# Kernel optimization log

Measured on AMD Instinct MI355X. Metric: run time of the kernel, lower is better.

Reference implementation:

```python
import jax, jax.numpy as jnp
import numpy as np

D = 64          # embed_dim
NH = 4          # nhead
DH = D // NH    # head dim
FF = 2048       # TransformerEncoderLayer default dim_feedforward
V = 1_000_000   # vocab (num items)
MAX_LEN = 50
INSERT_LEN = 10
EPS = 1e-5
N_LAYERS = 2


def setup_inputs() -> dict:
    key = jax.random.key(0)
    ks = jax.random.split(key, 8)
    s = 0.02
    return {
        "ht": jax.random.normal(ks[0], (D,), dtype=jnp.float32),
        "item_emb": jax.random.normal(ks[1], (V, D), dtype=jnp.float32) * s,
        "pos_emb": jax.random.normal(ks[2], (MAX_LEN, D), dtype=jnp.float32) * s,
        "in_proj_w": jax.random.normal(ks[3], (N_LAYERS, 3 * D, D), dtype=jnp.float32) * s,
        "in_proj_b": jnp.zeros((N_LAYERS, 3 * D), jnp.float32),
        "out_w": jax.random.normal(ks[4], (N_LAYERS, D, D), dtype=jnp.float32) * s,
        "out_b": jnp.zeros((N_LAYERS, D), jnp.float32),
        "ln1_w": jnp.ones((N_LAYERS, D), jnp.float32),
        "ln1_b": jnp.zeros((N_LAYERS, D), jnp.float32),
        "ln2_w": jnp.ones((N_LAYERS, D), jnp.float32),
        "ln2_b": jnp.zeros((N_LAYERS, D), jnp.float32),
        "ffn1_w": jax.random.normal(ks[5], (N_LAYERS, FF, D), dtype=jnp.float32) * s,
        "ffn1_b": jnp.zeros((N_LAYERS, FF), jnp.float32),
        "ffn2_w": jax.random.normal(ks[6], (N_LAYERS, D, FF), dtype=jnp.float32) * s,
        "ffn2_b": jnp.zeros((N_LAYERS, D), jnp.float32),
    }


def _ln(x, w, b):
    m = jnp.mean(x, axis=-1, keepdims=True)
    v = jnp.mean(jnp.square(x - m), axis=-1, keepdims=True)
    return (x - m) * jax.lax.rsqrt(v + EPS) * w + b


def _encoder_layer(x, ipw, ipb, ow, ob, l1w, l1b, l2w, l2b, f1w, f1b, f2w, f2b):
    # x: [S, D]; post-norm TransformerEncoderLayer (PyTorch defaults, eval mode)
    S = x.shape[0]
    qkv = x @ ipw.T + ipb                      # [S, 3D]
    q, k, v = jnp.split(qkv, 3, axis=-1)
    q = q.reshape(S, NH, DH)
    k = k.reshape(S, NH, DH)
    v = v.reshape(S, NH, DH)
    scores = jnp.einsum('shd,thd->hst', q, k) / jnp.sqrt(jnp.float32(DH))
    attn = jax.nn.softmax(scores, axis=-1)
    o = jnp.einsum('hst,thd->shd', attn, v).reshape(S, D)
    o = o @ ow.T + ob
    x = _ln(x + o, l1w, l1b)
    ff = jax.nn.relu(x @ f1w.T + f1b) @ f2w.T + f2b
    return _ln(x + ff, l2w, l2b)


def reference(ht, item_emb, pos_emb, in_proj_w, in_proj_b, out_w, out_b,
              ln1_w, ln1_b, ln2_w, ln2_b, ffn1_w, ffn1_b, ffn2_w, ffn2_b):
    gen = []         # generated item indices (traced int scalars)
    logits_all = []
    for _ in range(INSERT_LEN):
        if gen:
            gen_embed = item_emb[jnp.stack(gen)]             # [t, D]
            stack = jnp.concatenate([ht[None, :], gen_embed], axis=0)
        else:
            stack = ht[None, :]
        S = stack.shape[0]
        x = stack + pos_emb[:S]
        for l in range(N_LAYERS):
            x = _encoder_layer(x, in_proj_w[l], in_proj_b[l], out_w[l], out_b[l],
                               ln1_w[l], ln1_b[l], ln2_w[l], ln2_b[l],
                               ffn1_w[l], ffn1_b[l], ffn2_w[l], ffn2_b[l])
        logits = x[-1] @ item_emb.T                           # [V]
        gen.append(jnp.argmax(logits))
        logits_all.append(logits)
    return jnp.stack(logits_all), jnp.stack(gen)
```

## Files before the change

### kernel.cpp

```cpp
#include <hip/hip_runtime.h>

typedef unsigned long long u64;
typedef unsigned int u32;
typedef unsigned short u16;

#define V_ 1000000
#define STEPS_ 10
#define EPS_ 1e-5f
#define MARGIN_ 0.02f

__device__ __forceinline__ u64 pack_best(float v, int idx) {
    u32 u = __float_as_uint(v);
    u = (u & 0x80000000u) ? ~u : (u | 0x80000000u);
    return ((u64)u << 32) | (u64)(~(u32)idx);
}
__device__ __forceinline__ int unpack_idx(u64 p) { return (int)(~(u32)p); }
__device__ __forceinline__ float unpack_val(u64 p) {
    u32 hi = (u32)(p >> 32);
    return __uint_as_float((hi & 0x80000000u) ? (hi ^ 0x80000000u) : ~hi);
}
__device__ __forceinline__ u64 shfl_xor_u64(u64 v, int m) {
    u32 lo = (u32)v, hi = (u32)(v >> 32);
    lo = (u32)__shfl_xor((int)lo, m);
    hi = (u32)__shfl_xor((int)hi, m);
    return ((u64)hi << 32) | lo;
}
__device__ __forceinline__ u16 f2bf(float f) {
    u32 u = __float_as_uint(f);
    u += 0x7fffu + ((u >> 16) & 1u);
    return (u16)(u >> 16);
}
__device__ __forceinline__ float bf_lo(u32 u) { return __uint_as_float(u << 16); }
__device__ __forceinline__ float bf_hi(u32 u) { return __uint_as_float(u & 0xffff0000u); }

__device__ int resolve_argmax(const u64* __restrict__ cand,
                              const float* __restrict__ item_emb,
                              const float* __restrict__ y_last,
                              const float* __restrict__ lnw,
                              const float* __restrict__ lnb,
                              float* s_xl, int* s_list, u64* s_wm,
                              int* s_cnt, u64* s_best)
{
    const int tid = threadIdx.x;
    if (tid < 64) {
        float v = y_last[tid];
        float m = v;
        #pragma unroll
        for (int o = 1; o < 64; o <<= 1) m += __shfl_xor(m, o);
        m *= (1.f / 64.f);
        float df = v - m;
        float var = df * df;
        #pragma unroll
        for (int o = 1; o < 64; o <<= 1) var += __shfl_xor(var, o);
        var *= (1.f / 64.f);
        s_xl[tid] = df * (1.f / sqrtf(var + EPS_)) * lnw[tid] + lnb[tid];
    }
    if (tid == 0) { *s_cnt = 0; *s_best = 0ull; }
    __syncthreads();

    u64 m = 0ull;
    for (int i = tid; i < 2048; i += 256) { u64 c = cand[i]; if (c > m) m = c; }
    #pragma unroll
    for (int o = 1; o < 64; o <<= 1) { u64 x = shfl_xor_u64(m, o); if (x > m) m = x; }
    if ((tid & 63) == 0) s_wm[tid >> 6] = m;
    __syncthreads();
    if (tid == 0) {
        u64 b = s_wm[0];
        for (int i = 1; i < 4; i++) if (s_wm[i] > b) b = s_wm[i];
        s_wm[0] = b;
    }
    __syncthreads();

    float thr = unpack_val(s_wm[0]) - MARGIN_;
    for (int i = tid; i < 2048; i += 256) {
        if (unpack_val(cand[i]) >= thr) {
            int p = atomicAdd(s_cnt, 1);
            if (p < 64) s_list[p] = unpack_idx(cand[i]);
        }
    }
    __syncthreads();
    int n = *s_cnt; if (n > 64) n = 64;
    const int wid = tid >> 6, lane = tid & 63;
    for (int c = wid; c < n; c += 4) {
        int row = s_list[c];
        float p = s_xl[lane] * item_emb[(size_t)row * 64 + lane];
        #pragma unroll
        for (int o = 1; o < 64; o <<= 1) p += __shfl_xor(p, o);
        if (lane == 0) atomicMax(s_best, pack_best(p, row));
    }
    __syncthreads();
    return unpack_idx(*s_best);
}

__global__ __launch_bounds__(256) void attn0_kernel(
    const float* __restrict__ ht, const float* __restrict__ item_emb,
    const float* __restrict__ pos_emb,
    const float* __restrict__ ipw, const float* __restrict__ ipb,
    const float* __restrict__ ow,  const float* __restrict__ ob,
    const float* __restrict__ l1w, const float* __restrict__ l1b,
    const float* __restrict__ l2w1, const float* __restrict__ l2b1,
    const u64* __restrict__ cand, const float* __restrict__ y_last,
    int* __restrict__ gen_idx, float* __restrict__ gen_out,
    const float* __restrict__ f1w, const float* __restrict__ f1b,
    float* __restrict__ xp0, float* __restrict__ hbuf, int t)
{
    const int S = t + 1;
    const int tid = threadIdx.x;
    __shared__ float x[640], qkv[1920], att[400], o_[640], y2[640], xps[640];
    __shared__ float rm[10], rr[10], xl[64];
    __shared__ int list[64], cnt;
    __shared__ u64 wm[4], best;

    int newidx = -1;
    if (t > 0) {
        newidx = resolve_argmax(cand, item_emb, y_last, l2w1, l2b1,
                                xl, list, wm, &cnt, &best);
        if (blockIdx.x == 0 && tid == 0) {
            gen_idx[t - 1] = newidx;
            gen_out[t - 1] = (float)newidx;
        }
    }
    __syncthreads();

    for (int i = tid; i < S * 64; i += 256) {
        int s = i >> 6, d = i & 63;
        float base;
        if (s == 0) base = ht[d];
        else {
            int gi = (s == t) ? newidx : gen_idx[s - 1];
            base = item_emb[(size_t)gi * 64 + d];
        }
        x[i] = base + pos_emb[i];
    }
    __syncthreads();

    for (int i = tid; i < S * 192; i += 256) {
        int s = i / 192, j = i % 192;
        float acc = ipb[j];
        const float4* wr = (const float4*)(ipw + j * 64);
        const float4* xr = (const float4*)(x + s * 64);
        #pragma unroll
        for (int k = 0; k < 16; k++) {
            float4 w4 = wr[k], xv = xr[k];
            acc += w4.x * xv.x + w4.y * xv.y + w4.z * xv.z + w4.w * xv.w;
        }
        qkv[i] = acc;
    }
    __syncthreads();

    for (int i = tid; i < 4 * S * S; i += 256) {
        int h = i / (S * S), r = i % (S * S);
        int si = r / S, ti = r % S;
        const float* qr = qkv + si * 192 + h * 16;
        const float* kr = qkv + ti * 192 + 64 + h * 16;
        float acc = 0.f;
        #pragma unroll
        for (int k = 0; k < 16; k++) acc += qr[k] * kr[k];
        att[(h * S + si) * S + ti] = acc * 0.25f;
    }
    __syncthreads();

    for (int i = tid; i < 4 * S; i += 256) {
        float* row = att + i * S;
        float mx = row[0];
        for (int j = 1; j < S; j++) mx = fmaxf(mx, row[j]);
        float sm = 0.f;
        for (int j = 0; j < S; j++) { float e = expf(row[j] - mx); row[j] = e; sm += e; }
        float inv = 1.f / sm;
        for (int j = 0; j < S; j++) row[j] *= inv;
    }
    __syncthreads();

    for (int i = tid; i < S * 64; i += 256) {
        int si = i >> 6, d = i & 63, h = d >> 4, dh = d & 15;
        const float* ar = att + (h * S + si) * S;
        float acc = 0.f;
        for (int ti = 0; ti < S; ti++) acc += ar[ti] * qkv[ti * 192 + 128 + h * 16 + dh];
        o_[i] = acc;
    }
    __syncthreads();

    for (int i = tid; i < S * 64; i += 256) {
        int s = i >> 6, d = i & 63;
        float acc = ob[d] + x[i];
        const float4* wr = (const float4*)(ow + d * 64);
        const float4* orow = (const float4*)(o_ + s * 64);
        #pragma unroll
        for (int k = 0; k < 16; k++) {
            float4 w4 = wr[k], ov = orow[k];
            acc += w4.x * ov.x + w4.y * ov.y + w4.z * ov.z + w4.w * ov.w;
        }
        y2[i] = acc;
    }
    __syncthreads();

    if (tid < S) {
        const float* yr = y2 + tid * 64;
        float m = 0.f;
        for (int k = 0; k < 64; k++) m += yr[k];
        m *= (1.f / 64.f);
        float v = 0.f;
        for (int k = 0; k < 64; k++) { float df = yr[k] - m; v += df * df; }
        rm[tid] = m;
        rr[tid] = 1.f / sqrtf(v * (1.f / 64.f) + EPS_);
    }
    __syncthreads();
    for (int i = tid; i < S * 64; i += 256) {
        int s = i >> 6, d = i & 63;
        float v = (y2[i] - rm[s]) * rr[s] * l1w[d] + l1b[d];
        xps[i] = v;
        xp0[i] = v;
    }
    __syncthreads();

    const int jl = tid >> 4, kp = tid & 15;
    const int j = blockIdx.x * 16 + jl;
    float4 w4 = ((const float4*)(f1w + (size_t)j * 64))[kp];
    float b1 = f1b[j];
    for (int s = 0; s < S; s++) {
        float4 xv = ((const float4*)(xps + s * 64))[kp];
        float p = w4.x * xv.x + w4.y * xv.y + w4.z * xv.z + w4.w * xv.w;
        p += __shfl_xor(p, 1);
        p += __shfl_xor(p, 2);
        p += __shfl_xor(p, 4);
        p += __shfl_xor(p, 8);
        if (kp == 0) hbuf[s * 2048 + j] = fmaxf(p + b1, 0.f);
    }
}

__global__ __launch_bounds__(256) void ffn2_full_kernel(
    const float* __restrict__ f2w0, const float* __restrict__ f2b0,
    const float* __restrict__ hbuf, const float* __restrict__ xp0,
    float* __restrict__ y0, int S)
{
    const int tid = threadIdx.x, d = blockIdx.x;
    const float4* w4 = (const float4*)(f2w0 + (size_t)d * 2048 + tid * 8);
    float4 w0 = w4[0], w1 = w4[1];
    __shared__ float sw[4][10];
    for (int s = 0; s < S; s++) {
        const float4* h4 = (const float4*)(hbuf + s * 2048 + tid * 8);
        float4 h0 = h4[0], h1 = h4[1];
        float p = w0.x * h0.x + w0.y * h0.y + w0.z * h0.z + w0.w * h0.w
                + w1.x * h1.x + w1.y * h1.y + w1.z * h1.z + w1.w * h1.w;
        #pragma unroll
        for (int o = 1; o < 64; o <<= 1) p += __shfl_xor(p, o);
        if ((tid & 63) == 0) sw[tid >> 6][s] = p;
    }
    __syncthreads();
    if (tid < S)
        y0[tid * 64 + d] = sw[0][tid] + sw[1][tid] + sw[2][tid] + sw[3][tid]
                         + f2b0[d] + xp0[tid * 64 + d];
}

__global__ __launch_bounds__(256) void attn1_kernel(
    const float* __restrict__ y0,
    const float* __restrict__ l2w0, const float* __restrict__ l2b0,
    const float* __restrict__ ipw1, const float* __restrict__ ipb1,
    const float* __restrict__ ow1,  const float* __restrict__ ob1,
    const float* __restrict__ l1w1, const float* __restrict__ l1b1,
    const float* __restrict__ f1w1, const float* __restrict__ f1b1,
    float* __restrict__ xp1_last, float* __restrict__ hbuf, int S)
{
    const int tid = threadIdx.x;
    __shared__ float y0s[640], x1[640], qkv[1920], att[40], ol[64], y2l[64], xpl[64];
    __shared__ float rm[10], rr[10];

    for (int i = tid; i < S * 64; i += 256) y0s[i] = y0[i];
    __syncthreads();
    if (tid < S) {
        const float* yr = y0s + tid * 64;
        float m = 0.f;
        for (int k = 0; k < 64; k++) m += yr[k];
        m *= (1.f / 64.f);
        float v = 0.f;
        for (int k = 0; k < 64; k++) { float df = yr[k] - m; v += df * df; }
        rm[tid] = m;
        rr[tid] = 1.f / sqrtf(v * (1.f / 64.f) + EPS_);
    }
    __syncthreads();
    for (int i = tid; i < S * 64; i += 256) {
        int s = i >> 6, d = i & 63;
        x1[i] = (y0s[i] - rm[s]) * rr[s] * l2w0[d] + l2b0[d];
    }
    __syncthreads();

    for (int i = tid; i < S * 192; i += 256) {
        int s = i / 192, j = i % 192;
        float acc = ipb1[j];
        const float4* wr = (const float4*)(ipw1 + j * 64);
        const float4* xr = (const float4*)(x1 + s * 64);
        #pragma unroll
        for (int k = 0; k < 16; k++) {
            float4 w4 = wr[k], xv = xr[k];
            acc += w4.x * xv.x + w4.y * xv.y + w4.z * xv.z + w4.w * xv.w;
        }
        qkv[i] = acc;
    }
    __syncthreads();

    for (int i = tid; i < 4 * S; i += 256) {
        int h = i / S, ti = i % S;
        const float* qr = qkv + (S - 1) * 192 + h * 16;
        const float* kr = qkv + ti * 192 + 64 + h * 16;
        float acc = 0.f;
        #pragma unroll
        for (int k = 0; k < 16; k++) acc += qr[k] * kr[k];
        att[h * S + ti] = acc * 0.25f;
    }
    __syncthreads();
    if (tid < 4) {
        float* row = att + tid * S;
        float mx = row[0];
        for (int j = 1; j < S; j++) mx = fmaxf(mx, row[j]);
        float sm = 0.f;
        for (int j = 0; j < S; j++) { float e = expf(row[j] - mx); row[j] = e; sm += e; }
        float inv = 1.f / sm;
        for (int j = 0; j < S; j++) row[j] *= inv;
    }
    __syncthreads();
    if (tid < 64) {
        int h = tid >> 4, dh = tid & 15;
        const float* ar = att + h * S;
        float acc = 0.f;
        for (int ti = 0; ti < S; ti++) acc += ar[ti] * qkv[ti * 192 + 128 + h * 16 + dh];
        ol[tid] = acc;
    }
    __syncthreads();
    if (tid < 64) {
        float acc = ob1[tid] + x1[(S - 1) * 64 + tid];
        const float* wr = ow1 + tid * 64;
        for (int k = 0; k < 64; k++) acc += ol[k] * wr[k];
        y2l[tid] = acc;
    }
    __syncthreads();
    if (tid < 64) {
        float v = y2l[tid];
        float m = v;
        #pragma unroll
        for (int o = 1; o < 64; o <<= 1) m += __shfl_xor(m, o);
        m *= (1.f / 64.f);
        float df = v - m;
        float var = df * df;
        #pragma unroll
        for (int o = 1; o < 64; o <<= 1) var += __shfl_xor(var, o);
        float r = 1.f / sqrtf(var * (1.f / 64.f) + EPS_);
        float xv = df * r * l1w1[tid] + l1b1[tid];
        xpl[tid] = xv;
        xp1_last[tid] = xv;
    }
    __syncthreads();

    const int jl = tid >> 4, kp = tid & 15;
    const int j = blockIdx.x * 16 + jl;
    float4 w4 = ((const float4*)(f1w1 + (size_t)j * 64))[kp];
    float4 xv = ((const float4*)xpl)[kp];
    float p = w4.x * xv.x + w4.y * xv.y + w4.z * xv.z + w4.w * xv.w;
    p += __shfl_xor(p, 1);
    p += __shfl_xor(p, 2);
    p += __shfl_xor(p, 4);
    p += __shfl_xor(p, 8);
    if (kp == 0) hbuf[j] = fmaxf(p + f1b1[j], 0.f);
}

__global__ __launch_bounds__(256) void ffn2_last_kernel(
    const float* __restrict__ f2w1, const float* __restrict__ f2b1,
    const float* __restrict__ hbuf, const float* __restrict__ xp1_last,
    float* __restrict__ y_last)
{
    const int tid = threadIdx.x, d = blockIdx.x;
    const float4* w4 = (const float4*)(f2w1 + (size_t)d * 2048 + tid * 8);
    const float4* h4 = (const float4*)(hbuf + tid * 8);
    float4 w0 = w4[0], w1 = w4[1], h0 = h4[0], h1 = h4[1];
    float p = w0.x * h0.x + w0.y * h0.y + w0.z * h0.z + w0.w * h0.w
            + w1.x * h1.x + w1.y * h1.y + w1.z * h1.z + w1.w * h1.w;
    #pragma unroll
    for (int o = 1; o < 64; o <<= 1) p += __shfl_xor(p, o);
    __shared__ float sw[4];
    if ((tid & 63) == 0) sw[tid >> 6] = p;
    __syncthreads();
    if (tid == 0) y_last[d] = sw[0] + sw[1] + sw[2] + sw[3] + f2b1[d] + xp1_last[d];
}

__global__ __launch_bounds__(256) void logits_f32_kernel(
    const float* __restrict__ item_emb, const float* __restrict__ y_last,
    const float* __restrict__ lnw, const float* __restrict__ lnb,
    float* __restrict__ out, u64* __restrict__ cand, u16* __restrict__ emb16)
{
    const int tid = threadIdx.x;
    __shared__ float xl[64];
    if (tid < 64) {
        float v = y_last[tid];
        float m = v;
        #pragma unroll
        for (int o = 1; o < 64; o <<= 1) m += __shfl_xor(m, o);
        m *= (1.f / 64.f);
        float df = v - m;
        float var = df * df;
        #pragma unroll
        for (int o = 1; o < 64; o <<= 1) var += __shfl_xor(var, o);
        float r = 1.f / sqrtf(var * (1.f / 64.f) + EPS_);
        xl[tid] = df * r * lnw[tid] + lnb[tid];
    }
    __syncthreads();

    const int l16 = tid & 15;
    float4 q = ((const float4*)xl)[l16];
    const int group0 = (blockIdx.x * 256 + tid) >> 4;
    const int ngroups = (gridDim.x * 256) >> 4;
    u64 lb = 0ull;

    for (int row = group0; row < V_; row += ngroups) {
        float4 e = ((const float4*)(item_emb + (size_t)row * 64))[l16];
        ushort4 us;
        us.x = f2bf(e.x); us.y = f2bf(e.y); us.z = f2bf(e.z); us.w = f2bf(e.w);
        *(ushort4*)(emb16 + (size_t)row * 64 + l16 * 4) = us;
        float p = q.x * e.x + q.y * e.y + q.z * e.z + q.w * e.w;
        p += __shfl_xor(p, 1);
        p += __shfl_xor(p, 2);
        p += __shfl_xor(p, 4);
        p += __shfl_xor(p, 8);
        if (l16 == 0) {
            out[row] = p;
            u64 pk = pack_best(p, row);
            if (pk > lb) lb = pk;
        }
    }
    #pragma unroll
    for (int o = 1; o < 64; o <<= 1) { u64 x = shfl_xor_u64(lb, o); if (x > lb) lb = x; }
    __shared__ u64 sb[4];
    if ((tid & 63) == 0) sb[tid >> 6] = lb;
    __syncthreads();
    if (tid == 0) {
        u64 b = sb[0];
        for (int i = 1; i < 4; i++) if (sb[i] > b) b = sb[i];
        cand[blockIdx.x] = b;
    }
}

__global__ __launch_bounds__(256) void logits_bf16_kernel(
    const u16* __restrict__ emb16, const float* __restrict__ y_last,
    const float* __restrict__ lnw, const float* __restrict__ lnb,
    float* __restrict__ out, u64* __restrict__ cand)
{
    const int tid = threadIdx.x;
    __shared__ float xl[64];
    if (tid < 64) {
        float v = y_last[tid];
        float m = v;
        #pragma unroll
        for (int o = 1; o < 64; o <<= 1) m += __shfl_xor(m, o);
        m *= (1.f / 64.f);
        float df = v - m;
        float var = df * df;
        #pragma unroll
        for (int o = 1; o < 64; o <<= 1) var += __shfl_xor(var, o);
        float r = 1.f / sqrtf(var * (1.f / 64.f) + EPS_);
        xl[tid] = df * r * lnw[tid] + lnb[tid];
    }
    __syncthreads();

    const int j8 = tid & 7;
    float q[8];
    #pragma unroll
    for (int i = 0; i < 8; i++) q[i] = xl[j8 * 8 + i];
    const int group0 = (blockIdx.x * 256 + tid) >> 3;
    const int ngroups = (gridDim.x * 256) >> 3;
    const uint4* base = (const uint4*)emb16;
    u64 lb = 0ull;

    for (int row = group0; row < V_; row += ngroups) {
        uint4 u = base[(size_t)row * 8 + j8];
        float p = q[0] * bf_lo(u.x) + q[1] * bf_hi(u.x)
                + q[2] * bf_lo(u.y) + q[3] * bf_hi(u.y)
                + q[4] * bf_lo(u.z) + q[5] * bf_hi(u.z)
                + q[6] * bf_lo(u.w) + q[7] * bf_hi(u.w);
        p += __shfl_xor(p, 1);
        p += __shfl_xor(p, 2);
        p += __shfl_xor(p, 4);
        if (j8 == 0) {
            out[row] = p;
            u64 pk = pack_best(p, row);
            if (pk > lb) lb = pk;
        }
    }
    #pragma unroll
    for (int o = 1; o < 64; o <<= 1) { u64 x = shfl_xor_u64(lb, o); if (x > lb) lb = x; }
    __shared__ u64 sb[4];
    if ((tid & 63) == 0) sb[tid >> 6] = lb;
    __syncthreads();
    if (tid == 0) {
        u64 b = sb[0];
        for (int i = 1; i < 4; i++) if (sb[i] > b) b = sb[i];
        cand[blockIdx.x] = b;
    }
}

__global__ __launch_bounds__(256) void finalize_kernel(
    const u64* __restrict__ cand, const float* __restrict__ item_emb,
    const float* __restrict__ y_last,
    const float* __restrict__ lnw, const float* __restrict__ lnb,
    float* __restrict__ gen_out)
{
    __shared__ float xl[64];
    __shared__ int list[64], cnt;
    __shared__ u64 wm[4], best;
    int r = resolve_argmax(cand, item_emb, y_last, lnw, lnb, xl, list, wm, &cnt, &best);
    if (threadIdx.x == 0) gen_out[STEPS_ - 1] = (float)r;
}

extern "C" void kernel_launch(void* const* d_in, const int* in_sizes, int n_in,
                              void* d_out, int out_size, void* d_ws, size_t ws_size,
                              hipStream_t stream) {
    const float* ht       = (const float*)d_in[0];
    const float* item_emb = (const float*)d_in[1];
    const float* pos_emb  = (const float*)d_in[2];
    const float* ipw      = (const float*)d_in[3];
    const float* ipb      = (const float*)d_in[4];
    const float* ow       = (const float*)d_in[5];
    const float* ob       = (const float*)d_in[6];
    const float* l1w      = (const float*)d_in[7];
    const float* l1b      = (const float*)d_in[8];
    const float* l2w      = (const float*)d_in[9];
    const float* l2b      = (const float*)d_in[10];
    const float* f1w      = (const float*)d_in[11];
    const float* f1b      = (const float*)d_in[12];
    const float* f2w      = (const float*)d_in[13];
    const float* f2b      = (const float*)d_in[14];

    float* out = (float*)d_out;
    char* ws = (char*)d_ws;
    int*   gen_idx = (int*)ws;
    float* xp0     = (float*)(ws + 64);
    float* xp1l    = (float*)(ws + 2624);
    float* y_last  = (float*)(ws + 2880);
    float* y0      = (float*)(ws + 3136);
    float* hbuf    = (float*)(ws + 8192);
    u64*   cand    = (u64*)(ws + 90112);
    u16*   emb16   = (u16*)(ws + 131072);
    float* gen_out = out + (size_t)STEPS_ * V_;

    for (int t = 0; t < STEPS_; t++) {
        const int S = t + 1;
        attn0_kernel<<<128, 256, 0, stream>>>(
            ht, item_emb, pos_emb, ipw, ipb, ow, ob, l1w, l1b,
            l2w + 64, l2b + 64, cand, y_last, gen_idx, gen_out,
            f1w, f1b, xp0, hbuf, t);
        ffn2_full_kernel<<<64, 256, 0, stream>>>(f2w, f2b, hbuf, xp0, y0, S);
        attn1_kernel<<<128, 256, 0, stream>>>(
            y0, l2w, l2b, ipw + 192 * 64, ipb + 192, ow + 64 * 64, ob + 64,
            l1w + 64, l1b + 64, f1w + 2048 * 64, f1b + 2048, xp1l, hbuf, S);
        ffn2_last_kernel<<<64, 256, 0, stream>>>(
            f2w + (size_t)64 * 2048, f2b + 64, hbuf, xp1l, y_last);
        if (t == 0)
            logits_f32_kernel<<<2048, 256, 0, stream>>>(
                item_emb, y_last, l2w + 64, l2b + 64, out, cand, emb16);
        else
            logits_bf16_kernel<<<2048, 256, 0, stream>>>(
                emb16, y_last, l2w + 64, l2b + 64, out + (size_t)t * V_, cand);
    }
    finalize_kernel<<<1, 256, 0, stream>>>(
        cand, item_emb, y_last, l2w + 64, l2b + 64, gen_out);
}
```

Baseline: 1.024 ms.

## Fuse per-step layers with grid barriers, FP8 argmax scan, defer exact logits

The four per-step transformer kernels are merged into one persistent step kernel that uses global atomic grid barriers between the FFN stages. Per-step argmax scanning now uses an FP8 copy of the embedding table with chunked candidate maxima and a wider margin, then recomputes in fp32 to resolve the winner. All ten fp32 logit rows are written in a single final pass over item_emb using the saved normalized queries, rather than a bf16 pass per step. This cuts launch overhead and the bytes read per step, but adds risks: the spin barrier relies on all 64 blocks being resident at once, and FP8 rounding error could change the chosen argmax.

```diff
diff --git a/kernel.cpp b/kernel.cpp
--- a/kernel.cpp
+++ b/kernel.cpp
@@ -2,12 +2,16 @@
 
 typedef unsigned long long u64;
 typedef unsigned int u32;
-typedef unsigned short u16;
 
 #define V_ 1000000
 #define STEPS_ 10
 #define EPS_ 1e-5f
-#define MARGIN_ 0.02f
+#define MARGIN_ 0.06f
+#define FP8_SCALE 2048.0f
+#define FP8_INV (1.0f / 2048.0f)
+#define NCH 8192
+#define CH 123
+#define NBLK 64
 
 __device__ __forceinline__ u64 pack_best(float v, int idx) {
     u32 u = __float_as_uint(v);
@@ -25,21 +29,42 @@
     hi = (u32)__shfl_xor((int)hi, m);
     return ((u64)hi << 32) | lo;
 }
-__device__ __forceinline__ u16 f2bf(float f) {
-    u32 u = __float_as_uint(f);
-    u += 0x7fffu + ((u >> 16) & 1u);
-    return (u16)(u >> 16);
-}
-__device__ __forceinline__ float bf_lo(u32 u) { return __uint_as_float(u << 16); }
-__device__ __forceinline__ float bf_hi(u32 u) { return __uint_as_float(u & 0xffff0000u); }
+
+#define FP8_DOT16(u, q, p) do { \
+    auto a0 = __builtin_amdgcn_cvt_pk_f32_fp8((u).x, false); \
+    auto a1 = __builtin_amdgcn_cvt_pk_f32_fp8((u).x, true);  \
+    auto b0 = __builtin_amdgcn_cvt_pk_f32_fp8((u).y, false); \
+    auto b1 = __builtin_amdgcn_cvt_pk_f32_fp8((u).y, true);  \
+    auto c0 = __builtin_amdgcn_cvt_pk_f32_fp8((u).z, false); \
+    auto c1 = __builtin_amdgcn_cvt_pk_f32_fp8((u).z, true);  \
+    auto d0 = __builtin_amdgcn_cvt_pk_f32_fp8((u).w, false); \
+    auto d1 = __builtin_amdgcn_cvt_pk_f32_fp8((u).w, true);  \
+    p = q[0]*a0[0] + q[1]*a0[1] + q[2]*a1[0] + q[3]*a1[1] \
+      + q[4]*b0[0] + q[5]*b0[1] + q[6]*b1[0] + q[7]*b1[1] \
+      + q[8]*c0[0] + q[9]*c0[1] + q[10]*c1[0] + q[11]*c1[1] \
+      + q[12]*d0[0] + q[13]*d0[1] + q[14]*d1[0] + q[15]*d1[1]; \
+} while (0)
+
+__device__ __forceinline__ void grid_bar(u32* ctr, u32 expect) {
+    __threadfence();
+    __syncthreads();
+    if (threadIdx.x == 0) {
+        __hip_atomic_fetch_add(ctr, 1u, __ATOMIC_ACQ_REL, __HIP_MEMORY_SCOPE_AGENT);
+        while (__hip_atomic_load(ctr, __ATOMIC_ACQUIRE, __HIP_MEMORY_SCOPE_AGENT) < expect)
+            __builtin_amdgcn_s_sleep(2);
+    }
+    __syncthreads();
+    __threadfence();
+}
 
 __device__ int resolve_argmax(const u64* __restrict__ cand,
+                              const u32* __restrict__ emb8,
                               const float* __restrict__ item_emb,
                               const float* __restrict__ y_last,
                               const float* __restrict__ lnw,
                               const float* __restrict__ lnb,
-                              float* s_xl, int* s_list, u64* s_wm,
-                              int* s_cnt, u64* s_best)
+                              float* s_xl, int* s_list, int* s_qg, u64* s_wm,
+                              int* s_cnt, int* s_qcnt, u64* s_best)
 {
     const int tid = threadIdx.x;
     if (tid < 64) {
@@ -55,11 +80,11 @@
         var *= (1.f / 64.f);
         s_xl[tid] = df * (1.f / sqrtf(var + EPS_)) * lnw[tid] + lnb[tid];
     }
-    if (tid == 0) { *s_cnt = 0; *s_best = 0ull; }
+    if (tid == 0) { *s_cnt = 0; *s_qcnt = 0; *s_best = 0ull; }
     __syncthreads();
 
     u64 m = 0ull;
-    for (int i = tid; i < 2048; i += 256) { u64 c = cand[i]; if (c > m) m = c; }
+    for (int i = tid; i < NCH; i += 256) { u64 c = cand[i]; if (c > m) m = c; }
     #pragma unroll
     for (int o = 1; o < 64; o <<= 1) { u64 x = shfl_xor_u64(m, o); if (x > m) m = x; }
     if ((tid & 63) == 0) s_wm[tid >> 6] = m;
@@ -70,16 +95,45 @@
         s_wm[0] = b;
     }
     __syncthreads();
-
-    float thr = unpack_val(s_wm[0]) - MARGIN_;
-    for (int i = tid; i < 2048; i += 256) {
+    const float thr = unpack_val(s_wm[0]) - MARGIN_;
+
+    for (int i = tid; i < NCH; i += 256) {
         if (unpack_val(cand[i]) >= thr) {
-            int p = atomicAdd(s_cnt, 1);
-            if (p < 64) s_list[p] = unpack_idx(cand[i]);
-        }
-    }
-    __syncthreads();
-    int n = *s_cnt; if (n > 64) n = 64;
+            int p = atomicAdd(s_qcnt, 1);
+            if (p < 64) s_qg[p] = i;
+        }
+    }
+    __syncthreads();
+    int nq = *s_qcnt; if (nq > 64) nq = 64;
+
+    {
+        const int l4 = tid & 3, rl = tid >> 2;
+        float q[16];
+        #pragma unroll
+        for (int i = 0; i < 16; i++) q[i] = s_xl[l4 * 16 + i] * FP8_INV;
+        for (int ci = 0; ci < nq; ci++) {
+            const int r0 = s_qg[ci] * CH;
+            #pragma unroll
+            for (int half = 0; half < 2; half++) {
+                int loc = half * 64 + rl;
+                int row = r0 + loc;
+                if (loc < CH && row < V_) {
+                    uint4 u = ((const uint4*)emb8)[(size_t)row * 4 + l4];
+                    float p;
+                    FP8_DOT16(u, q, p);
+                    p += __shfl_xor(p, 1);
+                    p += __shfl_xor(p, 2);
+                    if (l4 == 0 && p >= thr - 1e-3f) {
+                        int pp = atomicAdd(s_cnt, 1);
+                        if (pp < 128) s_list[pp] = row;
+                    }
+                }
+            }
+        }
+    }
+    __syncthreads();
+    int n = *s_cnt; if (n > 128) n = 128;
+
     const int wid = tid >> 6, lane = tid & 63;
     for (int c = wid; c < n; c += 4) {
         int row = s_list[c];
@@ -92,33 +146,41 @@
     return unpack_idx(*s_best);
 }
 
-__global__ __launch_bounds__(256) void attn0_kernel(
+__global__ __launch_bounds__(256) void step_kernel(
     const float* __restrict__ ht, const float* __restrict__ item_emb,
     const float* __restrict__ pos_emb,
     const float* __restrict__ ipw, const float* __restrict__ ipb,
-    const float* __restrict__ ow,  const float* __restrict__ ob,
+    const float* __restrict__ ow, const float* __restrict__ ob,
     const float* __restrict__ l1w, const float* __restrict__ l1b,
-    const float* __restrict__ l2w1, const float* __restrict__ l2b1,
-    const u64* __restrict__ cand, const float* __restrict__ y_last,
+    const float* __restrict__ l2w, const float* __restrict__ l2b,
+    const float* __restrict__ f1w, const float* __restrict__ f1b,
+    const float* __restrict__ f2w, const float* __restrict__ f2b,
+    const u64* __restrict__ cand, const u32* __restrict__ emb8,
+    float* __restrict__ y_last,
     int* __restrict__ gen_idx, float* __restrict__ gen_out,
-    const float* __restrict__ f1w, const float* __restrict__ f1b,
-    float* __restrict__ xp0, float* __restrict__ hbuf, int t)
+    float* __restrict__ y0, float* __restrict__ hbuf, float* __restrict__ hbuf2,
+    u32* __restrict__ bar, int t)
 {
     const int S = t + 1;
-    const int tid = threadIdx.x;
-    __shared__ float x[640], qkv[1920], att[400], o_[640], y2[640], xps[640];
-    __shared__ float rm[10], rr[10], xl[64];
-    __shared__ int list[64], cnt;
+    const int tid = threadIdx.x, bid = blockIdx.x;
+    __shared__ __align__(16) float x[640], qkv[1920], o_[640], y2[640], xps[640];
+    __shared__ __align__(16) float xpl[64];
+    __shared__ float att[400], rm[10], rr[10], sw[4][10], xl[64], ol[64], y2l[64];
+    __shared__ int list[128], qg[64], cnt, qcnt;
     __shared__ u64 wm[4], best;
+
+    const float* ipw1 = ipw + 192 * 64;  const float* ipb1 = ipb + 192;
+    const float* ow1  = ow + 64 * 64;    const float* ob1  = ob + 64;
+    const float* l1w1 = l1w + 64;        const float* l1b1 = l1b + 64;
+    const float* l2w1 = l2w + 64;        const float* l2b1 = l2b + 64;
+    const float* f1w1 = f1w + 2048 * 64; const float* f1b1 = f1b + 2048;
+    const float* f2w1 = f2w + (size_t)64 * 2048; const float* f2b1 = f2b + 64;
 
     int newidx = -1;
     if (t > 0) {
-        newidx = resolve_argmax(cand, item_emb, y_last, l2w1, l2b1,
-                                xl, list, wm, &cnt, &best);
-        if (blockIdx.x == 0 && tid == 0) {
-            gen_idx[t - 1] = newidx;
-            gen_out[t - 1] = (float)newidx;
-        }
+        newidx = resolve_argmax(cand, emb8, item_emb, y_last, l2w1, l2b1,
+                                xl, list, qg, wm, &cnt, &qcnt, &best);
+        if (bid == 0 && tid == 0) { gen_idx[t - 1] = newidx; gen_out[t - 1] = (float)newidx; }
     }
     __syncthreads();
 
@@ -135,9 +197,9 @@
     __syncthreads();
 
     for (int i = tid; i < S * 192; i += 256) {
-        int s = i / 192, j = i % 192;
-        float acc = ipb[j];
-        const float4* wr = (const float4*)(ipw + j * 64);
+        int s = i / 192, j2 = i % 192;
+        float acc = ipb[j2];
+        const float4* wr = (const float4*)(ipw + j2 * 64);
         const float4* xr = (const float4*)(x + s * 64);
         #pragma unroll
         for (int k = 0; k < 16; k++) {
@@ -159,18 +221,16 @@
         att[(h * S + si) * S + ti] = acc * 0.25f;
     }
     __syncthreads();
-
     for (int i = tid; i < 4 * S; i += 256) {
         float* row = att + i * S;
         float mx = row[0];
-        for (int j = 1; j < S; j++) mx = fmaxf(mx, row[j]);
+        for (int j2 = 1; j2 < S; j2++) mx = fmaxf(mx, row[j2]);
         float sm = 0.f;
-        for (int j = 0; j < S; j++) { float e = expf(row[j] - mx); row[j] = e; sm += e; }
+        for (int j2 = 0; j2 < S; j2++) { float e = expf(row[j2] - mx); row[j2] = e; sm += e; }
         float inv = 1.f / sm;
-        for (int j = 0; j < S; j++) row[j] *= inv;
-    }
-    __syncthreads();
-
+        for (int j2 = 0; j2 < S; j2++) row[j2] *= inv;
+    }
+    __syncthreads();
     for (int i = tid; i < S * 64; i += 256) {
         int si = i >> 6, d = i & 63, h = d >> 4, dh = d & 15;
         const float* ar = att + (h * S + si) * S;
@@ -179,7 +239,6 @@
         o_[i] = acc;
     }
     __syncthreads();
-
     for (int i = tid; i < S * 64; i += 256) {
         int s = i >> 6, d = i & 63;
         float acc = ob[d] + x[i];
@@ -193,7 +252,6 @@
         y2[i] = acc;
     }
     __syncthreads();
-
     if (tid < S) {
         const float* yr = y2 + tid * 64;
         float m = 0.f;
@@ -207,68 +265,53 @@
     __syncthreads();
     for (int i = tid; i < S * 64; i += 256) {
         int s = i >> 6, d = i & 63;
-        float v = (y2[i] - rm[s]) * rr[s] * l1w[d] + l1b[d];
-        xps[i] = v;
-        xp0[i] = v;
-    }
-    __syncthreads();
-
-    const int jl = tid >> 4, kp = tid & 15;
-    const int j = blockIdx.x * 16 + jl;
-    float4 w4 = ((const float4*)(f1w + (size_t)j * 64))[kp];
-    float b1 = f1b[j];
-    for (int s = 0; s < S; s++) {
-        float4 xv = ((const float4*)(xps + s * 64))[kp];
-        float p = w4.x * xv.x + w4.y * xv.y + w4.z * xv.z + w4.w * xv.w;
-        p += __shfl_xor(p, 1);
-        p += __shfl_xor(p, 2);
-        p += __shfl_xor(p, 4);
-        p += __shfl_xor(p, 8);
-        if (kp == 0) hbuf[s * 2048 + j] = fmaxf(p + b1, 0.f);
-    }
-}
-
-__global__ __launch_bounds__(256) void ffn2_full_kernel(
-    const float* __restrict__ f2w0, const float* __restrict__ f2b0,
-    const float* __restrict__ hbuf, const float* __restrict__ xp0,
-    float* __restrict__ y0, int S)
-{
-    const int tid = threadIdx.x, d = blockIdx.x;
-    const float4* w4 = (const float4*)(f2w0 + (size_t)d * 2048 + tid * 8);
-    float4 w0 = w4[0], w1 = w4[1];
-    __shared__ float sw[4][10];
-    for (int s = 0; s < S; s++) {
-        const float4* h4 = (const float4*)(hbuf + s * 2048 + tid * 8);
-        float4 h0 = h4[0], h1 = h4[1];
-        float p = w0.x * h0.x + w0.y * h0.y + w0.z * h0.z + w0.w * h0.w
-                + w1.x * h1.x + w1.y * h1.y + w1.z * h1.z + w1.w * h1.w;
-        #pragma unroll
-        for (int o = 1; o < 64; o <<= 1) p += __shfl_xor(p, o);
-        if ((tid & 63) == 0) sw[tid >> 6][s] = p;
-    }
-    __syncthreads();
-    if (tid < S)
-        y0[tid * 64 + d] = sw[0][tid] + sw[1][tid] + sw[2][tid] + sw[3][tid]
-                         + f2b0[d] + xp0[tid * 64 + d];
-}
-
-__global__ __launch_bounds__(256) void attn1_kernel(
-    const float* __restrict__ y0,
-    const float* __restrict__ l2w0, const float* __restrict__ l2b0,
-    const float* __restrict__ ipw1, const float* __restrict__ ipb1,
-    const float* __restrict__ ow1,  const float* __restrict__ ob1,
-    const float* __restrict__ l1w1, const float* __restrict__ l1b1,
-    const float* __restrict__ f1w1, const float* __restrict__ f1b1,
-    float* __restrict__ xp1_last, float* __restrict__ hbuf, int S)
-{
-    const int tid = threadIdx.x;
-    __shared__ float y0s[640], x1[640], qkv[1920], att[40], ol[64], y2l[64], xpl[64];
-    __shared__ float rm[10], rr[10];
-
-    for (int i = tid; i < S * 64; i += 256) y0s[i] = y0[i];
+        xps[i] = (y2[i] - rm[s]) * rr[s] * l1w[d] + l1b[d];
+    }
+    __syncthreads();
+
+    const int jl = tid >> 3, kp = tid & 7;
+    const int j = bid * 32 + jl;
+    {
+        const float4* wr = (const float4*)(f1w + (size_t)j * 64);
+        float4 wa = wr[kp * 2], wb = wr[kp * 2 + 1];
+        float b1 = f1b[j];
+        for (int s = 0; s < S; s++) {
+            const float4* xr = (const float4*)(xps + s * 64);
+            float4 xa = xr[kp * 2], xb = xr[kp * 2 + 1];
+            float p = wa.x * xa.x + wa.y * xa.y + wa.z * xa.z + wa.w * xa.w
+                    + wb.x * xb.x + wb.y * xb.y + wb.z * xb.z + wb.w * xb.w;
+            p += __shfl_xor(p, 1);
+            p += __shfl_xor(p, 2);
+            p += __shfl_xor(p, 4);
+            if (kp == 0) hbuf[s * 2048 + j] = fmaxf(p + b1, 0.f);
+        }
+    }
+    grid_bar(bar + t * 4 + 0, NBLK);
+
+    {
+        const int d = bid;
+        const float4* w4 = (const float4*)(f2w + (size_t)d * 2048 + tid * 8);
+        float4 w0 = w4[0], w1 = w4[1];
+        for (int s = 0; s < S; s++) {
+            const float4* h4 = (const float4*)(hbuf + s * 2048 + tid * 8);
+            float4 h0 = h4[0], h1 = h4[1];
+            float p = w0.x * h0.x + w0.y * h0.y + w0.z * h0.z + w0.w * h0.w
+                    + w1.x * h1.x + w1.y * h1.y + w1.z * h1.z + w1.w * h1.w;
+            #pragma unroll
+            for (int o = 1; o < 64; o <<= 1) p += __shfl_xor(p, o);
+            if ((tid & 63) == 0) sw[tid >> 6][s] = p;
+        }
+        __syncthreads();
+        if (tid < S)
+            y0[tid * 64 + d] = sw[0][tid] + sw[1][tid] + sw[2][tid] + sw[3][tid]
+                             + f2b[d] + xps[tid * 64 + d];
+    }
+    grid_bar(bar + t * 4 + 1, NBLK);
+
+    for (int i = tid; i < S * 64; i += 256) y2[i] = y0[i];
     __syncthreads();
     if (tid < S) {
-        const float* yr = y0s + tid * 64;
+        const float* yr = y2 + tid * 64;
         float m = 0.f;
         for (int k = 0; k < 64; k++) m += yr[k];
         m *= (1.f / 64.f);
@@ -280,15 +323,15 @@
     __syncthreads();
     for (int i = tid; i < S * 64; i += 256) {
         int s = i >> 6, d = i & 63;
-        x1[i] = (y0s[i] - rm[s]) * rr[s] * l2w0[d] + l2b0[d];
+        x[i] = (y2[i] - rm[s]) * rr[s] * l2w[d] + l2b[d];
     }
     __syncthreads();
 
     for (int i = tid; i < S * 192; i += 256) {
-        int s = i / 192, j = i % 192;
-        float acc = ipb1[j];
-        const float4* wr = (const float4*)(ipw1 + j * 64);
-        const float4* xr = (const float4*)(x1 + s * 64);
+        int s = i / 192, j2 = i % 192;
+        float acc = ipb1[j2];
+        const float4* wr = (const float4*)(ipw1 + j2 * 64);
+        const float4* xr = (const float4*)(x + s * 64);
         #pragma unroll
         for (int k = 0; k < 16; k++) {
             float4 w4 = wr[k], xv = xr[k];
@@ -311,11 +354,11 @@
     if (tid < 4) {
         float* row = att + tid * S;
         float mx = row[0];
-        for (int j = 1; j < S; j++) mx = fmaxf(mx, row[j]);
+        for (int j2 = 1; j2 < S; j2++) mx = fmaxf(mx, row[j2]);
         float sm = 0.f;
-        for (int j = 0; j < S; j++) { float e = expf(row[j] - mx); row[j] = e; sm += e; }
+        for (int j2 = 0; j2 < S; j2++) { float e = expf(row[j2] - mx); row[j2] = e; sm += e; }
         float inv = 1.f / sm;
-        for (int j = 0; j < S; j++) row[j] *= inv;
+        for (int j2 = 0; j2 < S; j2++) row[j2] *= inv;
     }
     __syncthreads();
     if (tid < 64) {
@@ -327,7 +370,7 @@
     }
     __syncthreads();
     if (tid < 64) {
-        float acc = ob1[tid] + x1[(S - 1) * 64 + tid];
+        float acc = ob1[tid] + x[(S - 1) * 64 + tid];
         const float* wr = ow1 + tid * 64;
         for (int k = 0; k < 64; k++) acc += ol[k] * wr[k];
         y2l[tid] = acc;
@@ -344,47 +387,43 @@
         #pragma unroll
         for (int o = 1; o < 64; o <<= 1) var += __shfl_xor(var, o);
         float r = 1.f / sqrtf(var * (1.f / 64.f) + EPS_);
-        float xv = df * r * l1w1[tid] + l1b1[tid];
-        xpl[tid] = xv;
-        xp1_last[tid] = xv;
-    }
-    __syncthreads();
-
-    const int jl = tid >> 4, kp = tid & 15;
-    const int j = blockIdx.x * 16 + jl;
-    float4 w4 = ((const float4*)(f1w1 + (size_t)j * 64))[kp];
-    float4 xv = ((const float4*)xpl)[kp];
-    float p = w4.x * xv.x + w4.y * xv.y + w4.z * xv.z + w4.w * xv.w;
-    p += __shfl_xor(p, 1);
-    p += __shfl_xor(p, 2);
-    p += __shfl_xor(p, 4);
-    p += __shfl_xor(p, 8);
-    if (kp == 0) hbuf[j] = fmaxf(p + f1b1[j], 0.f);
-}
-
-__global__ __launch_bounds__(256) void ffn2_last_kernel(
-    const float* __restrict__ f2w1, const float* __restrict__ f2b1,
-    const float* __restrict__ hbuf, const float* __restrict__ xp1_last,
-    float* __restrict__ y_last)
-{
-    const int tid = threadIdx.x, d = blockIdx.x;
-    const float4* w4 = (const float4*)(f2w1 + (size_t)d * 2048 + tid * 8);
-    const float4* h4 = (const float4*)(hbuf + tid * 8);
-    float4 w0 = w4[0], w1 = w4[1], h0 = h4[0], h1 = h4[1];
-    float p = w0.x * h0.x + w0.y * h0.y + w0.z * h0.z + w0.w * h0.w
-            + w1.x * h1.x + w1.y * h1.y + w1.z * h1.z + w1.w * h1.w;
-    #pragma unroll
-    for (int o = 1; o < 64; o <<= 1) p += __shfl_xor(p, o);
-    __shared__ float sw[4];
-    if ((tid & 63) == 0) sw[tid >> 6] = p;
-    __syncthreads();
-    if (tid == 0) y_last[d] = sw[0] + sw[1] + sw[2] + sw[3] + f2b1[d] + xp1_last[d];
-}
-
-__global__ __launch_bounds__(256) void logits_f32_kernel(
+        xpl[tid] = df * r * l1w1[tid] + l1b1[tid];
+    }
+    __syncthreads();
+
+    {
+        const float4* wr = (const float4*)(f1w1 + (size_t)j * 64);
+        float4 wa = wr[kp * 2], wb = wr[kp * 2 + 1];
+        const float4* xr = (const float4*)xpl;
+        float4 xa = xr[kp * 2], xb = xr[kp * 2 + 1];
+        float p = wa.x * xa.x + wa.y * xa.y + wa.z * xa.z + wa.w * xa.w
+                + wb.x * xb.x + wb.y * xb.y + wb.z * xb.z + wb.w * xb.w;
+        p += __shfl_xor(p, 1);
+        p += __shfl_xor(p, 2);
+        p += __shfl_xor(p, 4);
+        if (kp == 0) hbuf2[j] = fmaxf(p + f1b1[j], 0.f);
+    }
+    grid_bar(bar + t * 4 + 2, NBLK);
+
+    {
+        const int d = bid;
+        const float4* w4 = (const float4*)(f2w1 + (size_t)d * 2048 + tid * 8);
+        const float4* h4 = (const float4*)(hbuf2 + tid * 8);
+        float4 w0 = w4[0], w1 = w4[1], h0 = h4[0], h1 = h4[1];
+        float p = w0.x * h0.x + w0.y * h0.y + w0.z * h0.z + w0.w * h0.w
+                + w1.x * h1.x + w1.y * h1.y + w1.z * h1.z + w1.w * h1.w;
+        #pragma unroll
+        for (int o = 1; o < 64; o <<= 1) p += __shfl_xor(p, o);
+        if ((tid & 63) == 0) sw[tid >> 6][0] = p;
+        __syncthreads();
+        if (tid == 0) y_last[d] = sw[0][0] + sw[1][0] + sw[2][0] + sw[3][0] + f2b1[d] + xpl[d];
+    }
+}
+
+__global__ __launch_bounds__(256) void scan0_kernel(
     const float* __restrict__ item_emb, const float* __restrict__ y_last,
     const float* __restrict__ lnw, const float* __restrict__ lnb,
-    float* __restrict__ out, u64* __restrict__ cand, u16* __restrict__ emb16)
+    u64* __restrict__ cand, float* __restrict__ xl_all, u32* __restrict__ emb8)
 {
     const int tid = threadIdx.x;
     __shared__ float xl[64];
@@ -399,51 +438,46 @@
         #pragma unroll
         for (int o = 1; o < 64; o <<= 1) var += __shfl_xor(var, o);
         float r = 1.f / sqrtf(var * (1.f / 64.f) + EPS_);
-        xl[tid] = df * r * lnw[tid] + lnb[tid];
-    }
-    __syncthreads();
-
-    const int l16 = tid & 15;
+        float v_ = df * r * lnw[tid] + lnb[tid];
+        xl[tid] = v_;
+        if (blockIdx.x == 0) xl_all[tid] = v_;
+    }
+    __syncthreads();
+
+    const int lane = tid & 63, wid = tid >> 6;
+    const int g = blockIdx.x * 4 + wid;
+    const int l16 = lane & 15, rl = lane >> 4;
     float4 q = ((const float4*)xl)[l16];
-    const int group0 = (blockIdx.x * 256 + tid) >> 4;
-    const int ngroups = (gridDim.x * 256) >> 4;
+    const int r0 = g * CH;
     u64 lb = 0ull;
-
-    for (int row = group0; row < V_; row += ngroups) {
-        float4 e = ((const float4*)(item_emb + (size_t)row * 64))[l16];
-        ushort4 us;
-        us.x = f2bf(e.x); us.y = f2bf(e.y); us.z = f2bf(e.z); us.w = f2bf(e.w);
-        *(ushort4*)(emb16 + (size_t)row * 64 + l16 * 4) = us;
-        float p = q.x * e.x + q.y * e.y + q.z * e.z + q.w * e.w;
-        p += __shfl_xor(p, 1);
-        p += __shfl_xor(p, 2);
-        p += __shfl_xor(p, 4);
-        p += __shfl_xor(p, 8);
-        if (l16 == 0) {
-            out[row] = p;
-            u64 pk = pack_best(p, row);
-            if (pk > lb) lb = pk;
+    for (int it = 0; it < 31; it++) {
+        int loc = it * 4 + rl;
+        int row = r0 + loc;
+        if (loc < CH && row < V_) {
+            float4 e = ((const float4*)(item_emb + (size_t)row * 64))[l16];
+            u32 pk8 = (u32)__builtin_amdgcn_cvt_pk_fp8_f32(e.x * FP8_SCALE, e.y * FP8_SCALE, 0, false);
+            pk8 = (u32)__builtin_amdgcn_cvt_pk_fp8_f32(e.z * FP8_SCALE, e.w * FP8_SCALE, (int)pk8, true);
+            emb8[(size_t)row * 16 + l16] = pk8;
+            float p = q.x * e.x + q.y * e.y + q.z * e.z + q.w * e.w;
+            p += __shfl_xor(p, 1);
+            p += __shfl_xor(p, 2);
+            p += __shfl_xor(p, 4);
+            p += __shfl_xor(p, 8);
+            if (l16 == 0) { u64 pk = pack_best(p, row); if (pk > lb) lb = pk; }
         }
     }
     #pragma unroll
-    for (int o = 1; o < 64; o <<= 1) { u64 x = shfl_xor_u64(lb, o); if (x > lb) lb = x; }
-    __shared__ u64 sb[4];
-    if ((tid & 63) == 0) sb[tid >> 6] = lb;
-    __syncthreads();
-    if (tid == 0) {
-        u64 b = sb[0];
-        for (int i = 1; i < 4; i++) if (sb[i] > b) b = sb[i];
-        cand[blockIdx.x] = b;
-    }
-}
-
-__global__ __launch_bounds__(256) void logits_bf16_kernel(
-    const u16* __restrict__ emb16, const float* __restrict__ y_last,
+    for (int o = 1; o < 64; o <<= 1) { u64 xv = shfl_xor_u64(lb, o); if (xv > lb) lb = xv; }
+    if (lane == 0) cand[g] = lb;
+}
+
+__global__ __launch_bounds__(256) void scan_fp8_kernel(
+    const u32* __restrict__ emb8, const float* __restrict__ y_last,
     const float* __restrict__ lnw, const float* __restrict__ lnb,
-    float* __restrict__ out, u64* __restrict__ cand)
+    u64* __restrict__ cand, float* __restrict__ xl_all, int t)
 {
     const int tid = threadIdx.x;
-    __shared__ float xl[64];
+    __shared__ float xls[64];
     if (tid < 64) {
         float v = y_last[tid];
         float m = v;
@@ -455,57 +489,87 @@
         #pragma unroll
         for (int o = 1; o < 64; o <<= 1) var += __shfl_xor(var, o);
         float r = 1.f / sqrtf(var * (1.f / 64.f) + EPS_);
-        xl[tid] = df * r * lnw[tid] + lnb[tid];
-    }
-    __syncthreads();
-
-    const int j8 = tid & 7;
-    float q[8];
+        float v_ = df * r * lnw[tid] + lnb[tid];
+        if (blockIdx.x == 0) xl_all[t * 64 + tid] = v_;
+        xls[tid] = v_ * FP8_INV;
+    }
+    __syncthreads();
+
+    const int lane = tid & 63, wid = tid >> 6;
+    const int g = blockIdx.x * 4 + wid;
+    const int l4 = lane & 3, rl = lane >> 2;
+    float q[16];
     #pragma unroll
-    for (int i = 0; i < 8; i++) q[i] = xl[j8 * 8 + i];
-    const int group0 = (blockIdx.x * 256 + tid) >> 3;
-    const int ngroups = (gridDim.x * 256) >> 3;
-    const uint4* base = (const uint4*)emb16;
+    for (int i = 0; i < 16; i++) q[i] = xls[l4 * 16 + i];
+    const int r0 = g * CH;
     u64 lb = 0ull;
-
-    for (int row = group0; row < V_; row += ngroups) {
-        uint4 u = base[(size_t)row * 8 + j8];
-        float p = q[0] * bf_lo(u.x) + q[1] * bf_hi(u.x)
-                + q[2] * bf_lo(u.y) + q[3] * bf_hi(u.y)
-                + q[4] * bf_lo(u.z) + q[5] * bf_hi(u.z)
-                + q[6] * bf_lo(u.w) + q[7] * bf_hi(u.w);
-        p += __shfl_xor(p, 1);
-        p += __shfl_xor(p, 2);
-        p += __shfl_xor(p, 4);
-        if (j8 == 0) {
-            out[row] = p;
-            u64 pk = pack_best(p, row);
-            if (pk > lb) lb = pk;
+    for (int it = 0; it < 8; it++) {
+        int loc = it * 16 + rl;
+        int row = r0 + loc;
+        if (loc < CH && row < V_) {
+            uint4 u = ((const uint4*)emb8)[(size_t)row * 4 + l4];
+            float p;
+            FP8_DOT16(u, q, p);
+            p += __shfl_xor(p, 1);
+            p += __shfl_xor(p, 2);
+            if (l4 == 0) { u64 pk = pack_best(p, row); if (pk > lb) lb = pk; }
         }
     }
     #pragma unroll
-    for (int o = 1; o < 64; o <<= 1) { u64 x = shfl_xor_u64(lb, o); if (x > lb) lb = x; }
-    __shared__ u64 sb[4];
-    if ((tid & 63) == 0) sb[tid >> 6] = lb;
-    __syncthreads();
-    if (tid == 0) {
-        u64 b = sb[0];
-        for (int i = 1; i < 4; i++) if (sb[i] > b) b = sb[i];
-        cand[blockIdx.x] = b;
-    }
+    for (int o = 1; o < 64; o <<= 1) { u64 xv = shfl_xor_u64(lb, o); if (xv > lb) lb = xv; }
+    if (lane == 0) cand[g] = lb;
 }
 
 __global__ __launch_bounds__(256) void finalize_kernel(
-    const u64* __restrict__ cand, const float* __restrict__ item_emb,
-    const float* __restrict__ y_last,
+    const u64* __restrict__ cand, const u32* __restrict__ emb8,
+    const float* __restrict__ item_emb, const float* __restrict__ y_last,
     const float* __restrict__ lnw, const float* __restrict__ lnb,
     float* __restrict__ gen_out)
 {
     __shared__ float xl[64];
-    __shared__ int list[64], cnt;
+    __shared__ int list[128], qg[64], cnt, qcnt;
     __shared__ u64 wm[4], best;
-    int r = resolve_argmax(cand, item_emb, y_last, lnw, lnb, xl, list, wm, &cnt, &best);
+    int r = resolve_argmax(cand, emb8, item_emb, y_last, lnw, lnb,
+                           xl, list, qg, wm, &cnt, &qcnt, &best);
     if (threadIdx.x == 0) gen_out[STEPS_ - 1] = (float)r;
+}
+
+__global__ __launch_bounds__(256) void logits_all_kernel(
+    const float* __restrict__ item_emb, const float* __restrict__ xl_all,
+    float* __restrict__ out)
+{
+    const int tid = threadIdx.x;
+    __shared__ __align__(16) float qs[640];
+    __shared__ float acc[640];
+    for (int i = tid; i < 640; i += 256) qs[i] = xl_all[i];
+    __syncthreads();
+    const int l16 = tid & 15, rl = tid >> 4;
+    float4 qv[10];
+    #pragma unroll
+    for (int t2 = 0; t2 < 10; t2++) qv[t2] = ((const float4*)(qs + t2 * 64))[l16];
+    for (int tile = blockIdx.x; tile < V_ / 64; tile += gridDim.x) {
+        const int base = tile * 64;
+        #pragma unroll
+        for (int sub = 0; sub < 4; sub++) {
+            const int r = sub * 16 + rl;
+            float4 e = ((const float4*)(item_emb + (size_t)(base + r) * 64))[l16];
+            #pragma unroll
+            for (int t2 = 0; t2 < 10; t2++) {
+                float p = qv[t2].x * e.x + qv[t2].y * e.y + qv[t2].z * e.z + qv[t2].w * e.w;
+                p += __shfl_xor(p, 1);
+                p += __shfl_xor(p, 2);
+                p += __shfl_xor(p, 4);
+                p += __shfl_xor(p, 8);
+                if (l16 == 0) acc[r * 10 + t2] = p;
+            }
+        }
+        __syncthreads();
+        for (int i = tid; i < 640; i += 256) {
+            int t2 = i >> 6, r = i & 63;
+            out[(size_t)t2 * V_ + base + r] = acc[r * 10 + t2];
+        }
+        __syncthreads();
+    }
 }
 
 extern "C" void kernel_launch(void* const* d_in, const int* in_sizes, int n_in,
@@ -530,34 +594,31 @@
     float* out = (float*)d_out;
     char* ws = (char*)d_ws;
     int*   gen_idx = (int*)ws;
-    float* xp0     = (float*)(ws + 64);
-    float* xp1l    = (float*)(ws + 2624);
-    float* y_last  = (float*)(ws + 2880);
-    float* y0      = (float*)(ws + 3136);
-    float* hbuf    = (float*)(ws + 8192);
-    u64*   cand    = (u64*)(ws + 90112);
-    u16*   emb16   = (u16*)(ws + 131072);
+    float* y_last  = (float*)(ws + 64);
+    float* y0      = (float*)(ws + 512);
+    float* hbuf2   = (float*)(ws + 3072);
+    float* xl_all  = (float*)(ws + 11264);
+    u32*   bar     = (u32*)(ws + 14336);
+    float* hbuf    = (float*)(ws + 16384);
+    u64*   cand    = (u64*)(ws + 131072);
+    u32*   emb8    = (u32*)(ws + 262144);
     float* gen_out = out + (size_t)STEPS_ * V_;
 
+    hipMemsetAsync(bar, 0, 256, stream);
+
     for (int t = 0; t < STEPS_; t++) {
-        const int S = t + 1;
-        attn0_kernel<<<128, 256, 0, stream>>>(
-            ht, item_emb, pos_emb, ipw, ipb, ow, ob, l1w, l1b,
-            l2w + 64, l2b + 64, cand, y_last, gen_idx, gen_out,
-            f1w, f1b, xp0, hbuf, t);
-        ffn2_full_kernel<<<64, 256, 0, stream>>>(f2w, f2b, hbuf, xp0, y0, S);
-        attn1_kernel<<<128, 256, 0, stream>>>(
-            y0, l2w, l2b, ipw + 192 * 64, ipb + 192, ow + 64 * 64, ob + 64,
-            l1w + 64, l1b + 64, f1w + 2048 * 64, f1b + 2048, xp1l, hbuf, S);
-        ffn2_last_kernel<<<64, 256, 0, stream>>>(
-            f2w + (size_t)64 * 2048, f2b + 64, hbuf, xp1l, y_last);
+        step_kernel<<<NBLK, 256, 0, stream>>>(
+            ht, item_emb, pos_emb, ipw, ipb, ow, ob, l1w, l1b, l2w, l2b,
+            f1w, f1b, f2w, f2b, cand, emb8, y_last, gen_idx, gen_out,
+            y0, hbuf, hbuf2, bar, t);
         if (t == 0)
-            logits_f32_kernel<<<2048, 256, 0, stream>>>(
-                item_emb, y_last, l2w + 64, l2b + 64, out, cand, emb16);
+            scan0_kernel<<<2048, 256, 0, stream>>>(
+                item_emb, y_last, l2w + 64, l2b + 64, cand, xl_all, emb8);
         else
-            logits_bf16_kernel<<<2048, 256, 0, stream>>>(
-                emb16, y_last, l2w + 64, l2b + 64, out + (size_t)t * V_, cand);
+            scan_fp8_kernel<<<2048, 256, 0, stream>>>(
+                emb8, y_last, l2w + 64, l2b + 64, cand, xl_all, t);
     }
     finalize_kernel<<<1, 256, 0, stream>>>(
-        cand, item_emb, y_last, l2w + 64, l2b + 64, gen_out);
-}
+        cand, emb8, item_emb, y_last, l2w + 64, l2b + 64, gen_out);
+    logits_all_kernel<<<2048, 256, 0, stream>>>(item_emb, xl_all, out);
+}
```

New measurement: 1.435 ms. 1.4x slower.
